# Performance work log

Measured on AMD Instinct MI355X. Metric: run time of the kernel, lower is better.

The kernel has to match this reference:

```python
import jax, jax.numpy as jnp
import numpy as np

B, D, H, E, TOP_K = 8192, 512, 2048, 8, 2


def setup_inputs() -> dict:
    key = jax.random.key(0)
    ks = jax.random.split(key, 7)
    s = 0.02
    return {
        "x": jax.random.normal(ks[0], (B, D), dtype=jnp.float32),
        "Wg": jax.random.normal(ks[1], (D, E), dtype=jnp.float32) * s,
        "bg": jnp.zeros((E,), dtype=jnp.float32),
        "W1": jax.random.normal(ks[2], (E, D, H), dtype=jnp.float32) * s,
        "b1": jnp.zeros((E, H), dtype=jnp.float32),
        "W2": jax.random.normal(ks[3], (E, H, D), dtype=jnp.float32) * s,
        "b2": jnp.zeros((E, D), dtype=jnp.float32),
    }


def reference(x, Wg, bg, W1, b1, W2, b2):
    # --- gating: top-k over expert logits, softmax over the k selected ---
    logits = x @ Wg + bg                                  # [B, E]
    top_v, top_i = jax.lax.top_k(logits, TOP_K)           # [B, K]
    w = jax.nn.softmax(top_v, axis=-1)                    # [B, K]
    # combine weights per expert: sum_k 1[top_i==e] * w   # [B, E]
    combine = jnp.sum(jax.nn.one_hot(top_i, E, dtype=x.dtype) * w[..., None], axis=1)
    # --- experts (dense-dispatch reference; zero combine weight == not routed,
    # so the math is identical to gather/compute/index_add of the original) ---
    h = jax.nn.gelu(jnp.einsum('bd,edh->ebh', x, W1) + b1[:, None, :],
                    approximate=False)                     # [E, B, H]
    y = jnp.einsum('ebh,ehd->ebd', h, W2) + b2[:, None, :] # [E, B, D]
    out = jnp.einsum('ebd,be->bd', y, combine)             # [B, D]
    return out, top_i
```

## Files before the change

### kernel.cpp

```cpp
#include <hip/hip_runtime.h>
#include <hip/hip_bf16.h>
#include <math.h>

#define B_TOK 8192
#define DIM   512
#define HID   2048
#define NE    8

#define BN 128
#define MAX_TILES 136
#define MAX_TILES64 272

typedef __attribute__((ext_vector_type(4))) float f32x4;
typedef __attribute__((ext_vector_type(8))) short short8;

typedef __attribute__((address_space(3))) unsigned int lds_u32_t;
typedef __attribute__((address_space(1))) unsigned int glob_u32_t;

__device__ __forceinline__ unsigned short f2bf(float f) {
  unsigned u = __builtin_bit_cast(unsigned, f);
  unsigned r = 0x7FFFu + ((u >> 16) & 1u);
  return (unsigned short)((u + r) >> 16);
}

__device__ __forceinline__ float bf2f(unsigned short u) {
  unsigned v = (unsigned)u << 16;
  return __builtin_bit_cast(float, v);
}

__device__ __forceinline__ void gld_lds16(const unsigned short* g, unsigned short* l) {
  __builtin_amdgcn_global_load_lds((const glob_u32_t*)g, (lds_u32_t*)l, 16, 0, 0);
}

__device__ __forceinline__ float gelu_fast(float x) {
  float u = x * (1.5957691216f + 0.0713548162f * x * x);
  float t = __expf(u);
  return x * t * __builtin_amdgcn_rcpf(t + 1.0f);
}

__global__ __launch_bounds__(256) void k_transpose2(const float* __restrict__ W1,
                                                    const float* __restrict__ W2,
                                                    unsigned short* __restrict__ w1t,
                                                    unsigned short* __restrict__ w2t) {
  __shared__ float tile[32][33];
  int z = blockIdx.z;
  const float* ine;
  unsigned short* oute;
  int R, C;
  if (z < NE) { ine = W1 + (size_t)z * DIM * HID; oute = w1t + (size_t)z * DIM * HID; R = DIM; C = HID; }
  else        { ine = W2 + (size_t)(z - NE) * HID * DIM; oute = w2t + (size_t)(z - NE) * HID * DIM; R = HID; C = DIM; }
  int Ct = C >> 5;
  int r0 = (blockIdx.x / Ct) * 32, c0 = (blockIdx.x % Ct) * 32;
  int tc = threadIdx.x & 31, tr = threadIdx.x >> 5;
#pragma unroll
  for (int i = 0; i < 4; ++i) {
    int r = tr + i * 8;
    tile[r][tc] = ine[(size_t)(r0 + r) * C + (c0 + tc)];
  }
  __syncthreads();
#pragma unroll
  for (int i = 0; i < 4; ++i) {
    int r = tr + i * 8;
    oute[(size_t)(c0 + r) * R + (r0 + tc)] = f2bf(tile[tc][r]);
  }
}

__global__ __launch_bounds__(256) void k_gate(const float* __restrict__ x,
                                              const float* __restrict__ Wg,
                                              const float* __restrict__ bg,
                                              float* __restrict__ topi,
                                              unsigned short* __restrict__ xbf,
                                              int* __restrict__ pairTok,
                                              int* __restrict__ tokEP,
                                              float* __restrict__ tokW,
                                              int* __restrict__ cnt) {
  __shared__ float wgs[DIM * NE + 28];
  __shared__ double partial[32][8][9];
  __shared__ double bgs[NE];
  __shared__ int lcnt[NE], lbase[NE];
  int t = threadIdx.x;
  if (t < NE) { bgs[t] = (double)bg[t]; lcnt[t] = 0; }
  for (int i = t; i < DIM * NE; i += 256) wgs[i + ((i >> 9) << 2)] = Wg[i];
  __syncthreads();

  int tokLocal = t >> 3;
  int part = t & 7;
  int token = blockIdx.x * 32 + tokLocal;
  size_t xoff = (size_t)token * DIM + part * 64;
  const float4* xr = (const float4*)(x + xoff);
  ushort4* xw = (ushort4*)(xbf + xoff);

  double acc[NE];
#pragma unroll
  for (int e = 0; e < NE; ++e) acc[e] = 0.0;

#pragma unroll
  for (int j = 0; j < 16; ++j) {
    float4 xv4 = xr[j];
    ushort4 o;
    o.x = f2bf(xv4.x); o.y = f2bf(xv4.y); o.z = f2bf(xv4.z); o.w = f2bf(xv4.w);
    xw[j] = o;
    const float* wb = &wgs[part * 516 + (j * 4) * 8];
#pragma unroll
    for (int k = 0; k < 4; ++k) {
      double xv = (double)((const float*)&xv4)[k];
#pragma unroll
      for (int e = 0; e < NE; ++e) acc[e] += xv * (double)wb[k * 8 + e];
    }
  }

#pragma unroll
  for (int e = 0; e < NE; ++e) partial[tokLocal][part][e] = acc[e];
  __syncthreads();

  int i0 = 0, i1 = 0, ls0 = 0, ls1 = 0;
  float w0 = 0.f, w1 = 0.f;
  if (part == 0) {
    double lg[NE];
#pragma unroll
    for (int e = 0; e < NE; ++e) {
      double s = bgs[e];
#pragma unroll
      for (int p = 0; p < 8; ++p) s += partial[tokLocal][p][e];
      lg[e] = s;
    }
    for (int e = 1; e < NE; ++e) if (lg[e] > lg[i0]) i0 = e;
    i1 = (i0 == 0) ? 1 : 0;
    for (int e = i1 + 1; e < NE; ++e) if (e != i0 && lg[e] > lg[i1]) i1 = e;
    double ex = exp(lg[i1] - lg[i0]);
    w0 = (float)(1.0 / (1.0 + ex));
    w1 = (float)(ex / (1.0 + ex));
    topi[token * 2 + 0] = (float)i0;
    topi[token * 2 + 1] = (float)i1;
    ls0 = atomicAdd(&lcnt[i0], 1);
    ls1 = atomicAdd(&lcnt[i1], 1);
  }
  __syncthreads();
  if (t < NE) lbase[t] = atomicAdd(&cnt[t], lcnt[t]);
  __syncthreads();
  if (part == 0) {
    int s0 = lbase[i0] + ls0;
    int s1 = lbase[i1] + ls1;
    pairTok[i0 * B_TOK + s0] = token;
    pairTok[i1 * B_TOK + s1] = token;
    tokEP[token * 2 + 0] = (i0 << 16) | s0;  tokW[token * 2 + 0] = w0;
    tokEP[token * 2 + 1] = (i1 << 16) | s1;  tokW[token * 2 + 1] = w1;
  }
}

__global__ __launch_bounds__(256) void k_schedule(const int* __restrict__ cnt,
                                                  int* __restrict__ numTiles,
                                                  int4* __restrict__ tileInfo,
                                                  int4* __restrict__ tileInfo64,
                                                  int* __restrict__ sBase,
                                                  int* __restrict__ pairTok) {
  __shared__ int sc[NE], spc[NE];
  int t = threadIdx.x;
  if (t == 0) {
    int off = 0, nt = 0, nt64 = 0;
    for (int e = 0; e < NE; ++e) {
      int c = cnt[e];
      sc[e] = c;
      int tl = (c + 127) >> 7;
      spc[e] = tl << 7;
      sBase[e] = off;
      for (int lt = 0; lt < tl; ++lt)
        tileInfo[nt++] = make_int4(e, e * B_TOK + lt * 128, off + lt * 128, 0);
      for (int lt = 0; lt < tl * 2; ++lt)
        tileInfo64[nt64++] = make_int4(e, off + lt * 64, 0, 0);
      off += tl << 7;
    }
    numTiles[0] = nt;
    numTiles[1] = nt64;
  }
  __syncthreads();
  for (int e = 0; e < NE; ++e)
    for (int i = sc[e] + t; i < spc[e]; i += 256)
      pairTok[e * B_TOK + i] = 0;
}

__global__ __launch_bounds__(512, 6) void k_gemm1(const unsigned short* __restrict__ xbf,
                                               const unsigned short* __restrict__ w1t,
                                               const float* __restrict__ b1,
                                               const int4* __restrict__ tileInfo,
                                               const int* __restrict__ numTiles,
                                               const int* __restrict__ pairTok,
                                               unsigned short* __restrict__ hbuf) {
  int L = blockIdx.y * 16 + blockIdx.x;
  int xcd = L & 7, o = L >> 3;
  int tile = xcd * 17 + (o >> 4);
  int n0 = (o & 15) * BN;
  if (tile >= numTiles[0]) return;
  int4 info = tileInfo[tile];
  int e = info.x, pairBase = info.y, slotBase = info.z;
  __shared__ unsigned short As[2][4096];
  __shared__ unsigned short Bs[2][4096];
  __shared__ int toks[128];
  int t = threadIdx.x;
  if (t < 128) toks[t] = pairTok[pairBase + t];
  __syncthreads();
  int row = t & 127, g4 = t >> 7;
  const unsigned short* aSrc = xbf + (size_t)toks[row] * DIM + g4 * 8;
  const unsigned short* bSrc = w1t + ((size_t)e * HID + n0 + row) * DIM + g4 * 8;
  int wv = t >> 6, lane = t & 63;
  int g = lane >> 4, r16 = lane & 15;
  int wr = (wv >> 2) * 64, wc = (wv & 3) * 32;
  f32x4 acc[4][2];
#pragma unroll
  for (int mi = 0; mi < 4; ++mi)
#pragma unroll
    for (int ni = 0; ni < 2; ++ni) acc[mi][ni] = (f32x4){0.f, 0.f, 0.f, 0.f};

#define G1_STAGE(buf, k0)                          \
  {                                                \
    gld_lds16(aSrc + (k0), &As[buf][wv * 512]);    \
    gld_lds16(bSrc + (k0), &Bs[buf][wv * 512]);    \
  }

  G1_STAGE(0, 0);
  __syncthreads();

  for (int ks = 0; ks < 16; ++ks) {
    int cur = ks & 1;
    if (ks < 15) G1_STAGE(cur ^ 1, (ks + 1) * 32);
    short8 am[4], bn[2];
#pragma unroll
    for (int mi = 0; mi < 4; ++mi)
      am[mi] = *(const short8*)&As[cur][((g * 128) + wr + mi * 16 + r16) * 8];
#pragma unroll
    for (int ni = 0; ni < 2; ++ni)
      bn[ni] = *(const short8*)&Bs[cur][((g * 128) + wc + ni * 16 + r16) * 8];
#pragma unroll
    for (int mi = 0; mi < 4; ++mi)
#pragma unroll
      for (int ni = 0; ni < 2; ++ni)
        acc[mi][ni] = __builtin_amdgcn_mfma_f32_16x16x32_bf16(bn[ni], am[mi], acc[mi][ni], 0, 0, 0);
    __syncthreads();
  }
#undef G1_STAGE

#pragma unroll
  for (int mi = 0; mi < 4; ++mi) {
    int srow = wr + mi * 16 + r16;
    size_t base = (size_t)(slotBase + srow) * HID;
#pragma unroll
    for (int ni = 0; ni < 2; ++ni) {
      int col0 = n0 + wc + ni * 16 + g * 4;
      float4 b4 = *(const float4*)&b1[e * HID + col0];
      unsigned h0 = f2bf(gelu_fast(acc[mi][ni][0] + b4.x));
      unsigned h1 = f2bf(gelu_fast(acc[mi][ni][1] + b4.y));
      unsigned h2 = f2bf(gelu_fast(acc[mi][ni][2] + b4.z));
      unsigned h3 = f2bf(gelu_fast(acc[mi][ni][3] + b4.w));
      uint2 pk;
      pk.x = h0 | (h1 << 16);
      pk.y = h2 | (h3 << 16);
      *(uint2*)&hbuf[base + col0] = pk;
    }
  }
}

__global__ __launch_bounds__(256) void k_gemm2(const unsigned short* __restrict__ hbuf,
                                               const unsigned short* __restrict__ w2t,
                                               const float* __restrict__ b2,
                                               const int4* __restrict__ tileInfo64,
                                               const int* __restrict__ numTiles,
                                               unsigned short* __restrict__ ybuf) {
  int L = blockIdx.y * 8 + blockIdx.x;
  int xcd = L & 7, o = L >> 3;
  int tile = xcd * 34 + (o >> 3);
  int n0 = (o & 7) * 64;
  if (tile >= numTiles[1]) return;
  int4 info = tileInfo64[tile];
  int e = info.x, slotBase = info.y;
  __shared__ unsigned short As[2][4096];
  __shared__ unsigned short Bs[2][4096];
  int t = threadIdx.x;
  int wv = t >> 6, lane = t & 63;

  int sg = t & 7, srow = t >> 3;
  int sj = sg ^ (srow & 7);
  const unsigned short* aSrc0 = hbuf + (size_t)(slotBase + srow) * HID + sj * 8;
  const unsigned short* aSrc1 = hbuf + (size_t)(slotBase + srow + 32) * HID + sj * 8;
  const unsigned short* bSrc0 = w2t + ((size_t)e * DIM + n0 + srow) * HID + sj * 8;
  const unsigned short* bSrc1 = w2t + ((size_t)e * DIM + n0 + srow + 32) * HID + sj * 8;

  int g16 = lane >> 4, r16 = lane & 15;
  int wr = (wv >> 1) * 32, wc = (wv & 1) * 32;
  f32x4 acc[2][2];
#pragma unroll
  for (int mi = 0; mi < 2; ++mi)
#pragma unroll
    for (int ni = 0; ni < 2; ++ni) acc[mi][ni] = (f32x4){0.f, 0.f, 0.f, 0.f};

  gld_lds16(aSrc0, &As[0][wv * 512]);
  gld_lds16(aSrc1, &As[0][2048 + wv * 512]);
  gld_lds16(bSrc0, &Bs[0][wv * 512]);
  gld_lds16(bSrc1, &Bs[0][2048 + wv * 512]);
  __syncthreads();

  for (int ks = 0; ks < 32; ++ks) {
    int cur = ks & 1;
    if (ks < 31) {
      int nb = cur ^ 1;
      int k0n = (ks + 1) * 64;
      gld_lds16(aSrc0 + k0n, &As[nb][wv * 512]);
      gld_lds16(aSrc1 + k0n, &As[nb][2048 + wv * 512]);
      gld_lds16(bSrc0 + k0n, &Bs[nb][wv * 512]);
      gld_lds16(bSrc1 + k0n, &Bs[nb][2048 + wv * 512]);
    }
    short8 am[2][2], bn[2][2];
#pragma unroll
    for (int mi = 0; mi < 2; ++mi) {
      int rrow = wr + mi * 16 + r16;
#pragma unroll
      for (int kk = 0; kk < 2; ++kk) {
        int j = (kk * 4 + g16) ^ (rrow & 7);
        am[mi][kk] = *(const short8*)&As[cur][rrow * 64 + j * 8];
      }
    }
#pragma unroll
    for (int ni = 0; ni < 2; ++ni) {
      int rrow = wc + ni * 16 + r16;
#pragma unroll
      for (int kk = 0; kk < 2; ++kk) {
        int j = (kk * 4 + g16) ^ (rrow & 7);
        bn[ni][kk] = *(const short8*)&Bs[cur][rrow * 64 + j * 8];
      }
    }
#pragma unroll
    for (int mi = 0; mi < 2; ++mi)
#pragma unroll
      for (int ni = 0; ni < 2; ++ni)
#pragma unroll
        for (int kk = 0; kk < 2; ++kk)
          acc[mi][ni] = __builtin_amdgcn_mfma_f32_16x16x32_bf16(bn[ni][kk], am[mi][kk], acc[mi][ni], 0, 0, 0);
    __syncthreads();
  }

#pragma unroll
  for (int mi = 0; mi < 2; ++mi) {
    int srow2 = wr + mi * 16 + r16;
    size_t base = (size_t)(slotBase + srow2) * DIM;
#pragma unroll
    for (int ni = 0; ni < 2; ++ni) {
      int col0 = n0 + wc + ni * 16 + g16 * 4;
      float4 b4 = *(const float4*)&b2[e * DIM + col0];
      unsigned y0 = f2bf(acc[mi][ni][0] + b4.x);
      unsigned y1 = f2bf(acc[mi][ni][1] + b4.y);
      unsigned y2 = f2bf(acc[mi][ni][2] + b4.z);
      unsigned y3 = f2bf(acc[mi][ni][3] + b4.w);
      uint2 pk;
      pk.x = y0 | (y1 << 16);
      pk.y = y2 | (y3 << 16);
      *(uint2*)&ybuf[base + col0] = pk;
    }
  }
}

__global__ __launch_bounds__(256) void k_combine(const unsigned short* __restrict__ ybuf,
                                                 const int* __restrict__ tokEP,
                                                 const float* __restrict__ tokW,
                                                 const int* __restrict__ sBase,
                                                 float* __restrict__ out) {
  int gid = blockIdx.x * 256 + threadIdx.x;
  int token = gid >> 7;
  int c4 = (gid & 127) * 4;
  int ep0 = tokEP[token * 2], ep1 = tokEP[token * 2 + 1];
  float w0 = tokW[token * 2], w1 = tokW[token * 2 + 1];
  size_t s0 = (size_t)(sBase[ep0 >> 16] + (ep0 & 0xFFFF));
  size_t s1 = (size_t)(sBase[ep1 >> 16] + (ep1 & 0xFFFF));
  ushort4 a = *(const ushort4*)&ybuf[s0 * DIM + c4];
  ushort4 b = *(const ushort4*)&ybuf[s1 * DIM + c4];
  float4 o;
  o.x = w0 * bf2f(a.x) + w1 * bf2f(b.x);
  o.y = w0 * bf2f(a.y) + w1 * bf2f(b.y);
  o.z = w0 * bf2f(a.z) + w1 * bf2f(b.z);
  o.w = w0 * bf2f(a.w) + w1 * bf2f(b.w);
  ((float4*)out)[gid] = o;
}

extern "C" void kernel_launch(void* const* d_in, const int* in_sizes, int n_in,
                              void* d_out, int out_size, void* d_ws, size_t ws_size,
                              hipStream_t stream) {
  (void)in_sizes; (void)n_in; (void)out_size; (void)ws_size;
  const float* x  = (const float*)d_in[0];
  const float* Wg = (const float*)d_in[1];
  const float* bg = (const float*)d_in[2];
  const float* W1 = (const float*)d_in[3];
  const float* b1 = (const float*)d_in[4];
  const float* W2 = (const float*)d_in[5];
  const float* b2 = (const float*)d_in[6];
  float* out  = (float*)d_out;
  float* topi = out + (size_t)B_TOK * DIM;

  char* ws = (char*)d_ws;
  int*  cnt        = (int*)(ws + 0);
  int*  numTiles   = (int*)(ws + 64);
  int*  sBase      = (int*)(ws + 128);
  int4* tileInfo64 = (int4*)(ws + 256);
  int4* tileInfo   = (int4*)(ws + 8192);
  int*  pairTok    = (int*)(ws + 16384);
  int*  tokEP      = (int*)(ws + 16384 + 262144);
  float* tokW      = (float*)(ws + 16384 + 262144 + 65536);
  unsigned short* ybuf = (unsigned short*)(ws + (1u << 20));
  unsigned short* xbf  = (unsigned short*)(ws + (1u << 20));
  unsigned short* w1t  = (unsigned short*)(ws + (1u << 20) + 8388608);
  unsigned short* w2t  = (unsigned short*)(ws + (1u << 20) + 8388608 + 16777216);
  unsigned short* hbuf = (unsigned short*)(ws + (1u << 20) + 8388608 + 16777216 + 16777216);

  hipMemsetAsync(cnt, 0, 64, stream);

  k_transpose2<<<dim3(1024, 1, 16), 256, 0, stream>>>(W1, W2, w1t, w2t);
  k_gate<<<dim3(B_TOK / 32), 256, 0, stream>>>(x, Wg, bg, topi, xbf, pairTok, tokEP, tokW, cnt);
  k_schedule<<<dim3(1), 256, 0, stream>>>(cnt, numTiles, tileInfo, tileInfo64, sBase, pairTok);
  k_gemm1<<<dim3(16, MAX_TILES), 512, 0, stream>>>(xbf, w1t, b1, tileInfo, numTiles, pairTok, hbuf);
  k_gemm2<<<dim3(8, MAX_TILES64), 256, 0, stream>>>(hbuf, w2t, b2, tileInfo64, numTiles, ybuf);
  k_combine<<<dim3((B_TOK * DIM) / 1024), 256, 0, stream>>>(ybuf, tokEP, tokW, sBase, out);
}
```

Measured before the change: 223.9 us.

## Retile expert GEMM1 to 64x64 blocks with swizzled LDS and K=64 steps

GEMM1 moves from 128x128 tiles with 512 threads and K-steps of 32 to 64x64 tiles with 256 threads, K-steps of 64 and an XOR-swizzled LDS layout, matching the GEMM2 kernel. The schedule now emits a single 64-row tile list that both GEMMs share, with the pair base and slot base stored per tile. The aim is more blocks for better occupancy and load balance, plus fewer LDS bank conflicts. The cost is less operand reuse per tile, so more global and LDS traffic for each FLOP.

```diff
diff --git a/kernel.cpp b/kernel.cpp
--- a/kernel.cpp
+++ b/kernel.cpp
@@ -7,7 +7,6 @@
 #define HID   2048
 #define NE    8
 
-#define BN 128
 #define MAX_TILES 136
 #define MAX_TILES64 272
 
@@ -150,27 +149,23 @@
 
 __global__ __launch_bounds__(256) void k_schedule(const int* __restrict__ cnt,
                                                   int* __restrict__ numTiles,
-                                                  int4* __restrict__ tileInfo,
                                                   int4* __restrict__ tileInfo64,
                                                   int* __restrict__ sBase,
                                                   int* __restrict__ pairTok) {
   __shared__ int sc[NE], spc[NE];
   int t = threadIdx.x;
   if (t == 0) {
-    int off = 0, nt = 0, nt64 = 0;
+    int off = 0, nt64 = 0;
     for (int e = 0; e < NE; ++e) {
       int c = cnt[e];
       sc[e] = c;
       int tl = (c + 127) >> 7;
       spc[e] = tl << 7;
       sBase[e] = off;
-      for (int lt = 0; lt < tl; ++lt)
-        tileInfo[nt++] = make_int4(e, e * B_TOK + lt * 128, off + lt * 128, 0);
       for (int lt = 0; lt < tl * 2; ++lt)
-        tileInfo64[nt64++] = make_int4(e, off + lt * 64, 0, 0);
+        tileInfo64[nt64++] = make_int4(e, e * B_TOK + lt * 64, off + lt * 64, 0);
       off += tl << 7;
     }
-    numTiles[0] = nt;
     numTiles[1] = nt64;
   }
   __syncthreads();
@@ -179,73 +174,95 @@
       pairTok[e * B_TOK + i] = 0;
 }
 
-__global__ __launch_bounds__(512, 6) void k_gemm1(const unsigned short* __restrict__ xbf,
+__global__ __launch_bounds__(256) void k_gemm1(const unsigned short* __restrict__ xbf,
                                                const unsigned short* __restrict__ w1t,
                                                const float* __restrict__ b1,
-                                               const int4* __restrict__ tileInfo,
+                                               const int4* __restrict__ tileInfo64,
                                                const int* __restrict__ numTiles,
                                                const int* __restrict__ pairTok,
                                                unsigned short* __restrict__ hbuf) {
-  int L = blockIdx.y * 16 + blockIdx.x;
+  int L = blockIdx.y * 32 + blockIdx.x;
   int xcd = L & 7, o = L >> 3;
-  int tile = xcd * 17 + (o >> 4);
-  int n0 = (o & 15) * BN;
-  if (tile >= numTiles[0]) return;
-  int4 info = tileInfo[tile];
+  int tile = xcd * 34 + (o >> 5);
+  int n0 = (o & 31) * 64;
+  if (tile >= numTiles[1]) return;
+  int4 info = tileInfo64[tile];
   int e = info.x, pairBase = info.y, slotBase = info.z;
   __shared__ unsigned short As[2][4096];
   __shared__ unsigned short Bs[2][4096];
-  __shared__ int toks[128];
+  __shared__ int toks[64];
   int t = threadIdx.x;
-  if (t < 128) toks[t] = pairTok[pairBase + t];
-  __syncthreads();
-  int row = t & 127, g4 = t >> 7;
-  const unsigned short* aSrc = xbf + (size_t)toks[row] * DIM + g4 * 8;
-  const unsigned short* bSrc = w1t + ((size_t)e * HID + n0 + row) * DIM + g4 * 8;
+  if (t < 64) toks[t] = pairTok[pairBase + t];
+  __syncthreads();
   int wv = t >> 6, lane = t & 63;
-  int g = lane >> 4, r16 = lane & 15;
-  int wr = (wv >> 2) * 64, wc = (wv & 3) * 32;
-  f32x4 acc[4][2];
-#pragma unroll
-  for (int mi = 0; mi < 4; ++mi)
+
+  int sg = t & 7, srow = t >> 3;
+  int sj = sg ^ (srow & 7);
+  const unsigned short* aSrc0 = xbf + (size_t)toks[srow] * DIM + sj * 8;
+  const unsigned short* aSrc1 = xbf + (size_t)toks[srow + 32] * DIM + sj * 8;
+  const unsigned short* bSrc0 = w1t + ((size_t)e * HID + n0 + srow) * DIM + sj * 8;
+  const unsigned short* bSrc1 = w1t + ((size_t)e * HID + n0 + srow + 32) * DIM + sj * 8;
+
+  int g16 = lane >> 4, r16 = lane & 15;
+  int wr = (wv >> 1) * 32, wc = (wv & 1) * 32;
+  f32x4 acc[2][2];
+#pragma unroll
+  for (int mi = 0; mi < 2; ++mi)
 #pragma unroll
     for (int ni = 0; ni < 2; ++ni) acc[mi][ni] = (f32x4){0.f, 0.f, 0.f, 0.f};
 
-#define G1_STAGE(buf, k0)                          \
-  {                                                \
-    gld_lds16(aSrc + (k0), &As[buf][wv * 512]);    \
-    gld_lds16(bSrc + (k0), &Bs[buf][wv * 512]);    \
-  }
-
-  G1_STAGE(0, 0);
-  __syncthreads();
-
-  for (int ks = 0; ks < 16; ++ks) {
+  gld_lds16(aSrc0, &As[0][wv * 512]);
+  gld_lds16(aSrc1, &As[0][2048 + wv * 512]);
+  gld_lds16(bSrc0, &Bs[0][wv * 512]);
+  gld_lds16(bSrc1, &Bs[0][2048 + wv * 512]);
+  __syncthreads();
+
+  for (int ks = 0; ks < 8; ++ks) {
     int cur = ks & 1;
-    if (ks < 15) G1_STAGE(cur ^ 1, (ks + 1) * 32);
-    short8 am[4], bn[2];
-#pragma unroll
-    for (int mi = 0; mi < 4; ++mi)
-      am[mi] = *(const short8*)&As[cur][((g * 128) + wr + mi * 16 + r16) * 8];
-#pragma unroll
-    for (int ni = 0; ni < 2; ++ni)
-      bn[ni] = *(const short8*)&Bs[cur][((g * 128) + wc + ni * 16 + r16) * 8];
-#pragma unroll
-    for (int mi = 0; mi < 4; ++mi)
+    if (ks < 7) {
+      int nb = cur ^ 1;
+      int k0n = (ks + 1) * 64;
+      gld_lds16(aSrc0 + k0n, &As[nb][wv * 512]);
+      gld_lds16(aSrc1 + k0n, &As[nb][2048 + wv * 512]);
+      gld_lds16(bSrc0 + k0n, &Bs[nb][wv * 512]);
+      gld_lds16(bSrc1 + k0n, &Bs[nb][2048 + wv * 512]);
+    }
+    short8 am[2][2], bn[2][2];
+#pragma unroll
+    for (int mi = 0; mi < 2; ++mi) {
+      int rrow = wr + mi * 16 + r16;
+#pragma unroll
+      for (int kk = 0; kk < 2; ++kk) {
+        int j = (kk * 4 + g16) ^ (rrow & 7);
+        am[mi][kk] = *(const short8*)&As[cur][rrow * 64 + j * 8];
+      }
+    }
+#pragma unroll
+    for (int ni = 0; ni < 2; ++ni) {
+      int rrow = wc + ni * 16 + r16;
+#pragma unroll
+      for (int kk = 0; kk < 2; ++kk) {
+        int j = (kk * 4 + g16) ^ (rrow & 7);
+        bn[ni][kk] = *(const short8*)&Bs[cur][rrow * 64 + j * 8];
+      }
+    }
+#pragma unroll
+    for (int mi = 0; mi < 2; ++mi)
 #pragma unroll
       for (int ni = 0; ni < 2; ++ni)
-        acc[mi][ni] = __builtin_amdgcn_mfma_f32_16x16x32_bf16(bn[ni], am[mi], acc[mi][ni], 0, 0, 0);
+#pragma unroll
+        for (int kk = 0; kk < 2; ++kk)
+          acc[mi][ni] = __builtin_amdgcn_mfma_f32_16x16x32_bf16(bn[ni][kk], am[mi][kk], acc[mi][ni], 0, 0, 0);
     __syncthreads();
   }
-#undef G1_STAGE
-
-#pragma unroll
-  for (int mi = 0; mi < 4; ++mi) {
-    int srow = wr + mi * 16 + r16;
-    size_t base = (size_t)(slotBase + srow) * HID;
+
+#pragma unroll
+  for (int mi = 0; mi < 2; ++mi) {
+    int srow2 = wr + mi * 16 + r16;
+    size_t base = (size_t)(slotBase + srow2) * HID;
 #pragma unroll
     for (int ni = 0; ni < 2; ++ni) {
-      int col0 = n0 + wc + ni * 16 + g * 4;
+      int col0 = n0 + wc + ni * 16 + g16 * 4;
       float4 b4 = *(const float4*)&b1[e * HID + col0];
       unsigned h0 = f2bf(gelu_fast(acc[mi][ni][0] + b4.x));
       unsigned h1 = f2bf(gelu_fast(acc[mi][ni][1] + b4.y));
@@ -271,7 +288,7 @@
   int n0 = (o & 7) * 64;
   if (tile >= numTiles[1]) return;
   int4 info = tileInfo64[tile];
-  int e = info.x, slotBase = info.y;
+  int e = info.x, slotBase = info.z;
   __shared__ unsigned short As[2][4096];
   __shared__ unsigned short Bs[2][4096];
   int t = threadIdx.x;
@@ -398,7 +415,6 @@
   int*  numTiles   = (int*)(ws + 64);
   int*  sBase      = (int*)(ws + 128);
   int4* tileInfo64 = (int4*)(ws + 256);
-  int4* tileInfo   = (int4*)(ws + 8192);
   int*  pairTok    = (int*)(ws + 16384);
   int*  tokEP      = (int*)(ws + 16384 + 262144);
   float* tokW      = (float*)(ws + 16384 + 262144 + 65536);
@@ -412,8 +428,8 @@
 
   k_transpose2<<<dim3(1024, 1, 16), 256, 0, stream>>>(W1, W2, w1t, w2t);
   k_gate<<<dim3(B_TOK / 32), 256, 0, stream>>>(x, Wg, bg, topi, xbf, pairTok, tokEP, tokW, cnt);
-  k_schedule<<<dim3(1), 256, 0, stream>>>(cnt, numTiles, tileInfo, tileInfo64, sBase, pairTok);
-  k_gemm1<<<dim3(16, MAX_TILES), 512, 0, stream>>>(xbf, w1t, b1, tileInfo, numTiles, pairTok, hbuf);
+  k_schedule<<<dim3(1), 256, 0, stream>>>(cnt, numTiles, tileInfo64, sBase, pairTok);
+  k_gemm1<<<dim3(32, MAX_TILES64), 256, 0, stream>>>(xbf, w1t, b1, tileInfo64, numTiles, pairTok, hbuf);
   k_gemm2<<<dim3(8, MAX_TILES64), 256, 0, stream>>>(hbuf, w2t, b2, tileInfo64, numTiles, ybuf);
   k_combine<<<dim3((B_TOK * DIM) / 1024), 256, 0, stream>>>(ybuf, tokEP, tokW, sBase, out);
 }
```

Result: faster. 195.6 us (-12.7%).
